# Performance work log

Hardware: AMD Instinct MI355X
Metric: run time of the kernel (lower is better)

## Reference

```python
import jax, jax.numpy as jnp
import numpy as np

B, K, H, E = 16384, 5, 512, 512


def setup_inputs() -> dict:
    key = jax.random.key(0)
    ks = jax.random.split(key, 6)
    return {
        "query": jax.random.normal(ks[0], (B, H), dtype=jnp.float32),
        "topics": jax.random.normal(ks[1], (B, K, E), dtype=jnp.float32),
        "coverage_vector": jax.random.uniform(ks[2], (B, K), dtype=jnp.float32),
        "Ua": jax.random.normal(ks[3], (H, E), dtype=jnp.float32) * (1.0 / np.sqrt(E)),
        "Wa": jax.random.normal(ks[4], (H, H), dtype=jnp.float32) * (1.0 / np.sqrt(H)),
        "va_w": jax.random.normal(ks[5], (1, H), dtype=jnp.float32) * (1.0 / np.sqrt(H)),
        "va_b": jnp.zeros((1,), dtype=jnp.float32),
    }


def reference(query, topics, coverage_vector, Ua, Wa, va_w, va_b):
    # proj_key for all topics at once: [B, K, H]
    proj_keys = jnp.einsum("bke,he->bkh", topics, Ua)
    # Faithful to original: query is re-projected by Wa each loop iteration,
    # so step i uses Wa^(i+1) @ query.
    q = query
    scores = []
    for i in range(topics.shape[1]):  # K is small & fixed (topics)
        q = q @ Wa.T  # [B, H]
        s = jnp.tanh(q + proj_keys[:, i, :]) @ va_w.T + va_b  # [B, 1]
        scores.append(s[:, 0] * coverage_vector[:, i])  # [B]
    scores = jnp.stack(scores, axis=1)  # [B, K]
    alphas = jax.nn.softmax(scores, axis=1)  # [B, K]
    mt = jnp.einsum("bk,bke->be", alphas, topics)  # [B, E]
    return (mt, alphas)
```

## Files before the change

kernel.cpp:

```cpp
#include <hip/hip_runtime.h>
#include <hip/hip_bf16.h>
#include <stdint.h>

#define B_SZ 16384
#define K_SZ 5
#define H_SZ 512
#define E_SZ 512

typedef _Float16 f16;
typedef _Float16 f16x8 __attribute__((ext_vector_type(8)));
typedef float    f32x4 __attribute__((ext_vector_type(4)));

__device__ __forceinline__ void gload_lds16(const void* g, void* l) {
  __builtin_amdgcn_global_load_lds(
      (const __attribute__((address_space(1))) unsigned int*)g,
      (__attribute__((address_space(3))) unsigned int*)l, 16, 0, 0);
}

__global__ __launch_bounds__(256) void cvt_kernel(const float* __restrict__ src,
                                                  f16* __restrict__ dst, int n8) {
  int i = blockIdx.x * 256 + threadIdx.x;
  if (i >= n8) return;
  size_t o = (size_t)i * 8;
  float4 a = *(const float4*)(src + o);
  float4 b = *(const float4*)(src + o + 4);
  union { f16 h[8]; uint4 u; } u;
  u.h[0] = (f16)a.x; u.h[1] = (f16)a.y; u.h[2] = (f16)a.z; u.h[3] = (f16)a.w;
  u.h[4] = (f16)b.x; u.h[5] = (f16)b.y; u.h[6] = (f16)b.z; u.h[7] = (f16)b.w;
  *(uint4*)(dst + o) = u.u;
}

__global__ __launch_bounds__(256)
void prep_weights(const float* __restrict__ Wa, const float* __restrict__ Ua,
                  f16* __restrict__ Wbig0, f16* __restrict__ Ua_h,
                  f16* __restrict__ WaT) {
  const int t = threadIdx.x;
  int bb = blockIdx.x;
  if (bb < 128) {
    size_t o = ((size_t)bb * 256 + t) * 8;
    float4 a = *(const float4*)(Wa + o);
    float4 b = *(const float4*)(Wa + o + 4);
    union { f16 h[8]; uint4 u; } u;
    u.h[0] = (f16)a.x; u.h[1] = (f16)a.y; u.h[2] = (f16)a.z; u.h[3] = (f16)a.w;
    u.h[4] = (f16)b.x; u.h[5] = (f16)b.y; u.h[6] = (f16)b.z; u.h[7] = (f16)b.w;
    *(uint4*)(Wbig0 + o) = u.u;
  } else if (bb < 256) {
    size_t o = ((size_t)(bb - 128) * 256 + t) * 8;
    float4 a = *(const float4*)(Ua + o);
    float4 b = *(const float4*)(Ua + o + 4);
    union { f16 h[8]; uint4 u; } u;
    u.h[0] = (f16)a.x; u.h[1] = (f16)a.y; u.h[2] = (f16)a.z; u.h[3] = (f16)a.w;
    u.h[4] = (f16)b.x; u.h[5] = (f16)b.y; u.h[6] = (f16)b.z; u.h[7] = (f16)b.w;
    *(uint4*)(Ua_h + o) = u.u;
  } else {
    __shared__ float tile[32][33];
    int blk = bb - 256;
    int bx = blk & 15, by = blk >> 4;
    int tx = t & 31, ty = t >> 5;
    #pragma unroll
    for (int i = 0; i < 32; i += 8)
      tile[ty + i][tx] = Wa[(size_t)(by * 32 + ty + i) * 512 + bx * 32 + tx];
    __syncthreads();
    #pragma unroll
    for (int i = 0; i < 32; i += 8)
      WaT[(size_t)(bx * 32 + ty + i) * 512 + by * 32 + tx] =
          (f16)tile[tx][ty + i];
  }
}

template <bool A_F32>
__global__ __launch_bounds__(256)
void gemm_bt(const void* __restrict__ Aop, const f16* __restrict__ W,
             f16* __restrict__ Y, int ldA, int ldY, int nTn) {
  __shared__ f16 As[128 * 32];
  __shared__ f16 Bs[128 * 32];
  const int t = threadIdx.x;
  const int l = t & 63, wid = t >> 6;
  const int wm = wid >> 1, wn = wid & 1;
  int bid = blockIdx.x;
  const int nwg = gridDim.x;
  if ((nwg & 7) == 0) bid = (bid & 7) * (nwg >> 3) + (bid >> 3);
  const int n0 = (bid % nTn) * 128;
  const size_t m0 = (size_t)(bid / nTn) * 128;
  const int lrow = l & 15;
  const int lk = (l >> 4) * 8;

  f32x4 acc[4][4] = {};

  for (int k0 = 0; k0 < 512; k0 += 32) {
    #pragma unroll
    for (int p = 0; p < 2; ++p) {
      int c = p * 256 + t;
      int row = c >> 2, seg = c & 3;
      gload_lds16(W + (size_t)(n0 + row) * 512 + k0 + seg * 8,
                  (char*)Bs + c * 16);
    }
    if constexpr (!A_F32) {
      const f16* A = (const f16*)Aop;
      #pragma unroll
      for (int p = 0; p < 2; ++p) {
        int c = p * 256 + t;
        int row = c >> 2, seg = c & 3;
        gload_lds16(A + (m0 + row) * (size_t)ldA + k0 + seg * 8,
                    (char*)As + c * 16);
      }
    } else {
      const float* A = (const float*)Aop;
      #pragma unroll
      for (int p = 0; p < 4; ++p) {
        int c = p * 256 + t;
        int row = c >> 3, seg = c & 7;
        const float4 v =
            *(const float4*)(A + (m0 + row) * (size_t)ldA + k0 + seg * 4);
        union { f16 h[4]; uint2 u; } cv;
        cv.h[0] = (f16)v.x; cv.h[1] = (f16)v.y;
        cv.h[2] = (f16)v.z; cv.h[3] = (f16)v.w;
        *(uint2*)((char*)As + row * 64 + seg * 8) = cv.u;
      }
    }
    __syncthreads();

    f16x8 af[4], bf[4];
    #pragma unroll
    for (int mi = 0; mi < 4; ++mi)
      af[mi] = *(const f16x8*)(As + (wm * 64 + mi * 16 + lrow) * 32 + lk);
    #pragma unroll
    for (int ni = 0; ni < 4; ++ni)
      bf[ni] = *(const f16x8*)(Bs + (wn * 64 + ni * 16 + lrow) * 32 + lk);
    #pragma unroll
    for (int mi = 0; mi < 4; ++mi)
      #pragma unroll
      for (int ni = 0; ni < 4; ++ni)
        acc[mi][ni] = __builtin_amdgcn_mfma_f32_16x16x32_f16(
            af[mi], bf[ni], acc[mi][ni], 0, 0, 0);
    __syncthreads();
  }

  #pragma unroll
  for (int mi = 0; mi < 4; ++mi) {
    #pragma unroll
    for (int j = 0; j < 4; ++j) {
      size_t row = m0 + wm * 64 + mi * 16 + ((l >> 4) << 2) + j;
      #pragma unroll
      for (int ni = 0; ni < 4; ++ni) {
        int col = n0 + wn * 64 + ni * 16 + lrow;
        Y[row * (size_t)ldY + col] = (f16)acc[mi][ni][j];
      }
    }
  }
}

__device__ __forceinline__ float fast_tanh(float x) {
  float e = __expf(-2.f * fabsf(x));
  float r = (1.f - e) / (1.f + e);
  return copysignf(r, x);
}

__device__ __forceinline__ void softmax_mt_dev(size_t b, int l, const float* s,
                                               const float* __restrict__ topics,
                                               float* __restrict__ out) {
  float m = s[0];
  #pragma unroll
  for (int k = 1; k < K_SZ; ++k) m = fmaxf(m, s[k]);
  float a[K_SZ], d = 0.f;
  #pragma unroll
  for (int k = 0; k < K_SZ; ++k) { a[k] = __expf(s[k] - m); d += a[k]; }
  float inv = 1.f / d;
  #pragma unroll
  for (int k = 0; k < K_SZ; ++k) a[k] *= inv;

  float acc0[4] = {}, acc1[4] = {};
  #pragma unroll
  for (int k = 0; k < K_SZ; ++k) {
    const float* tp = topics + (b * K_SZ + k) * E_SZ + l * 8;
    float4 t0 = *(const float4*)tp;
    float4 t1 = *(const float4*)(tp + 4);
    acc0[0] += a[k] * t0.x; acc0[1] += a[k] * t0.y;
    acc0[2] += a[k] * t0.z; acc0[3] += a[k] * t0.w;
    acc1[0] += a[k] * t1.x; acc1[1] += a[k] * t1.y;
    acc1[2] += a[k] * t1.z; acc1[3] += a[k] * t1.w;
  }
  float* mo = out + b * E_SZ + l * 8;
  *(float4*)mo       = make_float4(acc0[0], acc0[1], acc0[2], acc0[3]);
  *(float4*)(mo + 4) = make_float4(acc1[0], acc1[1], acc1[2], acc1[3]);
  if (l < K_SZ) {
    float av = (l == 0) ? a[0] : (l == 1) ? a[1] : (l == 2) ? a[2]
               : (l == 3) ? a[3] : a[4];
    out[(size_t)B_SZ * E_SZ + b * K_SZ + l] = av;
  }
}

__global__ __launch_bounds__(256)
void finalize_full(const f16* __restrict__ qall, const f16* __restrict__ pk,
                   const float* __restrict__ topics, const float* __restrict__ cov,
                   const float* __restrict__ va_w, const float* __restrict__ va_b,
                   float* __restrict__ out) {
  const int wid = threadIdx.x >> 6, l = threadIdx.x & 63;
  const size_t b = (size_t)blockIdx.x * 4 + wid;
  const float vb = va_b[0];
  float va[8];
  *(float4*)(va)     = *(const float4*)(va_w + l * 8);
  *(float4*)(va + 4) = *(const float4*)(va_w + l * 8 + 4);

  float s[K_SZ];
  #pragma unroll
  for (int k = 0; k < K_SZ; ++k) {
    const size_t r = (b * K_SZ + k) * 512 + l * 8;
    f16x8 qv = *(const f16x8*)(qall + r);
    f16x8 pv = *(const f16x8*)(pk + r);
    float part = 0.f;
    #pragma unroll
    for (int j = 0; j < 8; ++j)
      part += va[j] * fast_tanh((float)qv[j] + (float)pv[j]);
    #pragma unroll
    for (int off = 32; off > 0; off >>= 1) part += __shfl_xor(part, off);
    s[k] = (part + vb) * cov[b * K_SZ + k];
  }
  softmax_mt_dev(b, l, s, topics, out);
}

extern "C" void kernel_launch(void* const* d_in, const int* in_sizes, int n_in,
                              void* d_out, int out_size, void* d_ws, size_t ws_size,
                              hipStream_t stream) {
  const float* query  = (const float*)d_in[0];
  const float* topics = (const float*)d_in[1];
  const float* cov    = (const float*)d_in[2];
  const float* Ua     = (const float*)d_in[3];
  const float* Wa     = (const float*)d_in[4];
  const float* va_w   = (const float*)d_in[5];
  const float* va_b   = (const float*)d_in[6];
  float* out = (float*)d_out;

  char* ws = (char*)d_ws;
  size_t off = 0;
  auto alloc = [&](size_t bytes) -> char* {
    char* p = ws + off;
    off += (bytes + 255) & ~(size_t)255;
    return p;
  };
  f16* q0h  = (f16*)alloc((size_t)B_SZ * H_SZ * 2);
  f16* qall = (f16*)alloc((size_t)B_SZ * K_SZ * H_SZ * 2);
  f16* Ua_h = (f16*)alloc((size_t)H_SZ * E_SZ * 2);
  f16* WaT  = (f16*)alloc((size_t)H_SZ * H_SZ * 2);
  f16* Wbig = (f16*)alloc((size_t)K_SZ * H_SZ * H_SZ * 2);
  f16* pk   = (f16*)alloc((size_t)B_SZ * K_SZ * H_SZ * 2);

  prep_weights<<<512, 256, 0, stream>>>(Wa, Ua, Wbig, Ua_h, WaT);
  cvt_kernel<<<B_SZ * H_SZ / 8 / 256, 256, 0, stream>>>(query, q0h,
                                                        B_SZ * H_SZ / 8);
  for (int j = 1; j < K_SZ; ++j)
    gemm_bt<false><<<16, 256, 0, stream>>>(
        Wbig + (size_t)(j - 1) * H_SZ * H_SZ, WaT,
        Wbig + (size_t)j * H_SZ * H_SZ, H_SZ, H_SZ, 4);
  gemm_bt<false><<<(B_SZ / 128) * (K_SZ * H_SZ / 128), 256, 0, stream>>>(
      q0h, Wbig, qall, H_SZ, K_SZ * H_SZ, K_SZ * H_SZ / 128);
  gemm_bt<true><<<(B_SZ * K_SZ / 128) * (H_SZ / 128), 256, 0, stream>>>(
      topics, Ua_h, pk, E_SZ, H_SZ, H_SZ / 128);
  finalize_full<<<B_SZ / 4, 256, 0, stream>>>(qall, pk, topics, cov, va_w,
                                              va_b, out);
}
```

Baseline: 486.4 us.

## Fuse key and query projection GEMMs with tanh-score epilogue into one kernel

Replaces the two separate GEMMs (query projection through stacked Wa powers, and topic projection through Ua) with one kernel. It accumulates both products into the same register tile per (topic, row-tile, column-tile), then applies tanh and the va dot product in the epilogue, writing per-slice partial scores. This removes the write and re-read of the two large fp16 intermediates (qall and pk). The trade-off is that a small finalize kernel must sum 8 partial slices per score, and each block now runs twice the K-loop length.

```diff
diff --git a/kernel.cpp b/kernel.cpp
--- a/kernel.cpp
+++ b/kernel.cpp
@@ -68,9 +68,8 @@
   }
 }
 
-template <bool A_F32>
 __global__ __launch_bounds__(256)
-void gemm_bt(const void* __restrict__ Aop, const f16* __restrict__ W,
+void gemm_bt(const f16* __restrict__ A, const f16* __restrict__ W,
              f16* __restrict__ Y, int ldA, int ldY, int nTn) {
   __shared__ f16 As[128 * 32];
   __shared__ f16 Bs[128 * 32];
@@ -94,29 +93,8 @@
       int row = c >> 2, seg = c & 3;
       gload_lds16(W + (size_t)(n0 + row) * 512 + k0 + seg * 8,
                   (char*)Bs + c * 16);
-    }
-    if constexpr (!A_F32) {
-      const f16* A = (const f16*)Aop;
-      #pragma unroll
-      for (int p = 0; p < 2; ++p) {
-        int c = p * 256 + t;
-        int row = c >> 2, seg = c & 3;
-        gload_lds16(A + (m0 + row) * (size_t)ldA + k0 + seg * 8,
-                    (char*)As + c * 16);
-      }
-    } else {
-      const float* A = (const float*)Aop;
-      #pragma unroll
-      for (int p = 0; p < 4; ++p) {
-        int c = p * 256 + t;
-        int row = c >> 3, seg = c & 7;
-        const float4 v =
-            *(const float4*)(A + (m0 + row) * (size_t)ldA + k0 + seg * 4);
-        union { f16 h[4]; uint2 u; } cv;
-        cv.h[0] = (f16)v.x; cv.h[1] = (f16)v.y;
-        cv.h[2] = (f16)v.z; cv.h[3] = (f16)v.w;
-        *(uint2*)((char*)As + row * 64 + seg * 8) = cv.u;
-      }
+      gload_lds16(A + (m0 + row) * (size_t)ldA + k0 + seg * 8,
+                  (char*)As + c * 16);
     }
     __syncthreads();
 
@@ -156,9 +134,138 @@
   return copysignf(r, x);
 }
 
-__device__ __forceinline__ void softmax_mt_dev(size_t b, int l, const float* s,
-                                               const float* __restrict__ topics,
-                                               float* __restrict__ out) {
+__global__ __launch_bounds__(256)
+void fused_score_gemm(const float* __restrict__ topics,
+                      const f16* __restrict__ q0h,
+                      const f16* __restrict__ Ua_h,
+                      const f16* __restrict__ Wbig,
+                      const float* __restrict__ va_w,
+                      float* __restrict__ partials) {
+  __shared__ f16 As[128 * 32];
+  __shared__ f16 Bs[128 * 32];
+  const int t = threadIdx.x;
+  const int l = t & 63, wid = t >> 6;
+  const int wm = wid >> 1, wn = wid & 1;
+  int bid = blockIdx.x;
+  const int nwg = gridDim.x;
+  bid = (bid & 7) * (nwg >> 3) + (bid >> 3);
+  const int k = bid >> 9;
+  const int rem = bid & 511;
+  const int mt = rem >> 2, nt = rem & 3;
+  const size_t m0 = (size_t)mt * 128;
+  const int n0 = nt * 128;
+  const int lrow = l & 15;
+  const int lk = (l >> 4) * 8;
+  const f16* Pk = Wbig + (size_t)k * 512 * 512;
+
+  f32x4 acc[4][4] = {};
+
+  for (int k0 = 0; k0 < 512; k0 += 32) {
+    #pragma unroll
+    for (int p = 0; p < 2; ++p) {
+      int c = p * 256 + t;
+      int row = c >> 2, seg = c & 3;
+      gload_lds16(Ua_h + (size_t)(n0 + row) * 512 + k0 + seg * 8,
+                  (char*)Bs + c * 16);
+    }
+    #pragma unroll
+    for (int p = 0; p < 4; ++p) {
+      int c = p * 256 + t;
+      int row = c >> 3, seg = c & 7;
+      const float4 v = *(const float4*)(
+          topics + ((m0 + row) * K_SZ + k) * E_SZ + k0 + seg * 4);
+      union { f16 h[4]; uint2 u; } cv;
+      cv.h[0] = (f16)v.x; cv.h[1] = (f16)v.y;
+      cv.h[2] = (f16)v.z; cv.h[3] = (f16)v.w;
+      *(uint2*)((char*)As + row * 64 + seg * 8) = cv.u;
+    }
+    __syncthreads();
+
+    f16x8 af[4], bf[4];
+    #pragma unroll
+    for (int mi = 0; mi < 4; ++mi)
+      af[mi] = *(const f16x8*)(As + (wm * 64 + mi * 16 + lrow) * 32 + lk);
+    #pragma unroll
+    for (int ni = 0; ni < 4; ++ni)
+      bf[ni] = *(const f16x8*)(Bs + (wn * 64 + ni * 16 + lrow) * 32 + lk);
+    #pragma unroll
+    for (int mi = 0; mi < 4; ++mi)
+      #pragma unroll
+      for (int ni = 0; ni < 4; ++ni)
+        acc[mi][ni] = __builtin_amdgcn_mfma_f32_16x16x32_f16(
+            af[mi], bf[ni], acc[mi][ni], 0, 0, 0);
+    __syncthreads();
+  }
+
+  for (int k0 = 0; k0 < 512; k0 += 32) {
+    #pragma unroll
+    for (int p = 0; p < 2; ++p) {
+      int c = p * 256 + t;
+      int row = c >> 2, seg = c & 3;
+      gload_lds16(Pk + (size_t)(n0 + row) * 512 + k0 + seg * 8,
+                  (char*)Bs + c * 16);
+      gload_lds16(q0h + (m0 + row) * (size_t)H_SZ + k0 + seg * 8,
+                  (char*)As + c * 16);
+    }
+    __syncthreads();
+
+    f16x8 af[4], bf[4];
+    #pragma unroll
+    for (int mi = 0; mi < 4; ++mi)
+      af[mi] = *(const f16x8*)(As + (wm * 64 + mi * 16 + lrow) * 32 + lk);
+    #pragma unroll
+    for (int ni = 0; ni < 4; ++ni)
+      bf[ni] = *(const f16x8*)(Bs + (wn * 64 + ni * 16 + lrow) * 32 + lk);
+    #pragma unroll
+    for (int mi = 0; mi < 4; ++mi)
+      #pragma unroll
+      for (int ni = 0; ni < 4; ++ni)
+        acc[mi][ni] = __builtin_amdgcn_mfma_f32_16x16x32_f16(
+            af[mi], bf[ni], acc[mi][ni], 0, 0, 0);
+    __syncthreads();
+  }
+
+  const int colbase = n0 + wn * 64 + lrow;
+  float va4[4];
+  #pragma unroll
+  for (int ni = 0; ni < 4; ++ni) va4[ni] = va_w[colbase + ni * 16];
+
+  #pragma unroll
+  for (int mi = 0; mi < 4; ++mi) {
+    #pragma unroll
+    for (int j = 0; j < 4; ++j) {
+      float s = 0.f;
+      #pragma unroll
+      for (int ni = 0; ni < 4; ++ni)
+        s += va4[ni] * fast_tanh(acc[mi][ni][j]);
+      #pragma unroll
+      for (int m = 1; m < 16; m <<= 1) s += __shfl_xor(s, m);
+      if (lrow == 0) {
+        int row = (int)m0 + wm * 64 + mi * 16 + ((l >> 4) << 2) + j;
+        partials[(size_t)(nt * 2 + wn) * (K_SZ * B_SZ) + k * B_SZ + row] = s;
+      }
+    }
+  }
+}
+
+__global__ __launch_bounds__(256)
+void finalize2(const float* __restrict__ partials,
+               const float* __restrict__ topics, const float* __restrict__ cov,
+               const float* __restrict__ va_b, float* __restrict__ out) {
+  const int wid = threadIdx.x >> 6, l = threadIdx.x & 63;
+  const size_t b = (size_t)blockIdx.x * 4 + wid;
+  const float vb = va_b[0];
+
+  float s[K_SZ];
+  #pragma unroll
+  for (int k = 0; k < K_SZ; ++k) {
+    float raw = 0.f;
+    #pragma unroll
+    for (int sl = 0; sl < 8; ++sl)
+      raw += partials[(size_t)sl * (K_SZ * B_SZ) + k * B_SZ + b];
+    s[k] = (raw + vb) * cov[b * K_SZ + k];
+  }
+
   float m = s[0];
   #pragma unroll
   for (int k = 1; k < K_SZ; ++k) m = fmaxf(m, s[k]);
@@ -188,35 +295,6 @@
                : (l == 3) ? a[3] : a[4];
     out[(size_t)B_SZ * E_SZ + b * K_SZ + l] = av;
   }
-}
-
-__global__ __launch_bounds__(256)
-void finalize_full(const f16* __restrict__ qall, const f16* __restrict__ pk,
-                   const float* __restrict__ topics, const float* __restrict__ cov,
-                   const float* __restrict__ va_w, const float* __restrict__ va_b,
-                   float* __restrict__ out) {
-  const int wid = threadIdx.x >> 6, l = threadIdx.x & 63;
-  const size_t b = (size_t)blockIdx.x * 4 + wid;
-  const float vb = va_b[0];
-  float va[8];
-  *(float4*)(va)     = *(const float4*)(va_w + l * 8);
-  *(float4*)(va + 4) = *(const float4*)(va_w + l * 8 + 4);
-
-  float s[K_SZ];
-  #pragma unroll
-  for (int k = 0; k < K_SZ; ++k) {
-    const size_t r = (b * K_SZ + k) * 512 + l * 8;
-    f16x8 qv = *(const f16x8*)(qall + r);
-    f16x8 pv = *(const f16x8*)(pk + r);
-    float part = 0.f;
-    #pragma unroll
-    for (int j = 0; j < 8; ++j)
-      part += va[j] * fast_tanh((float)qv[j] + (float)pv[j]);
-    #pragma unroll
-    for (int off = 32; off > 0; off >>= 1) part += __shfl_xor(part, off);
-    s[k] = (part + vb) * cov[b * K_SZ + k];
-  }
-  softmax_mt_dev(b, l, s, topics, out);
 }
 
 extern "C" void kernel_launch(void* const* d_in, const int* in_sizes, int n_in,
@@ -238,24 +316,20 @@
     off += (bytes + 255) & ~(size_t)255;
     return p;
   };
-  f16* q0h  = (f16*)alloc((size_t)B_SZ * H_SZ * 2);
-  f16* qall = (f16*)alloc((size_t)B_SZ * K_SZ * H_SZ * 2);
-  f16* Ua_h = (f16*)alloc((size_t)H_SZ * E_SZ * 2);
-  f16* WaT  = (f16*)alloc((size_t)H_SZ * H_SZ * 2);
-  f16* Wbig = (f16*)alloc((size_t)K_SZ * H_SZ * H_SZ * 2);
-  f16* pk   = (f16*)alloc((size_t)B_SZ * K_SZ * H_SZ * 2);
+  f16* q0h   = (f16*)alloc((size_t)B_SZ * H_SZ * 2);
+  f16* Ua_h  = (f16*)alloc((size_t)H_SZ * E_SZ * 2);
+  f16* WaT   = (f16*)alloc((size_t)H_SZ * H_SZ * 2);
+  f16* Wbig  = (f16*)alloc((size_t)K_SZ * H_SZ * H_SZ * 2);
+  float* partials = (float*)alloc((size_t)8 * K_SZ * B_SZ * 4);
 
   prep_weights<<<512, 256, 0, stream>>>(Wa, Ua, Wbig, Ua_h, WaT);
   cvt_kernel<<<B_SZ * H_SZ / 8 / 256, 256, 0, stream>>>(query, q0h,
                                                         B_SZ * H_SZ / 8);
   for (int j = 1; j < K_SZ; ++j)
-    gemm_bt<false><<<16, 256, 0, stream>>>(
-        Wbig + (size_t)(j - 1) * H_SZ * H_SZ, WaT,
-        Wbig + (size_t)j * H_SZ * H_SZ, H_SZ, H_SZ, 4);
-  gemm_bt<false><<<(B_SZ / 128) * (K_SZ * H_SZ / 128), 256, 0, stream>>>(
-      q0h, Wbig, qall, H_SZ, K_SZ * H_SZ, K_SZ * H_SZ / 128);
-  gemm_bt<true><<<(B_SZ * K_SZ / 128) * (H_SZ / 128), 256, 0, stream>>>(
-      topics, Ua_h, pk, E_SZ, H_SZ, H_SZ / 128);
-  finalize_full<<<B_SZ / 4, 256, 0, stream>>>(qall, pk, topics, cov, va_w,
-                                              va_b, out);
-}
+    gemm_bt<<<16, 256, 0, stream>>>(Wbig + (size_t)(j - 1) * H_SZ * H_SZ, WaT,
+                                    Wbig + (size_t)j * H_SZ * H_SZ, H_SZ,
+                                    H_SZ, 4);
+  fused_score_gemm<<<K_SZ * (B_SZ / 128) * (H_SZ / 128), 256, 0, stream>>>(
+      topics, q0h, Ua_h, Wbig, va_w, partials);
+  finalize2<<<B_SZ / 4, 256, 0, stream>>>(partials, topics, cov, va_b, out);
+}
```

New measurement: 464.5 us. 4.5% less time.
